# Optimization experiments

Hardware: AMD Instinct MI355X
Metric: run time of the kernel (lower is better)

## Reference

```python
import jax, jax.numpy as jnp
import numpy as np
import math

B, C, L = 8, 128, 8192
MODES = 512
TIME_DIM = 256
HIDDEN = 352  # SwiGLU: int(2*4*128/3)=341 rounded up to multiple of 16
EPS = 1e-6


def setup_inputs() -> dict:
    key = jax.random.key(0)
    ks = jax.random.split(key, 16)
    scale = 1.0 / (C * C)
    return {
        "x": jax.random.normal(ks[0], (B, C, L), jnp.float32),
        "t_emb": jax.random.normal(ks[1], (B, TIME_DIM), jnp.float32),
        "w_real": scale * jax.random.normal(ks[2], (C, C, MODES), jnp.float32),
        "w_imag": scale * jax.random.normal(ks[3], (C, C, MODES), jnp.float32),
        "shifts": 0.05 * jax.random.normal(ks[4], (C,), jnp.float32),
        "pw_w": jax.random.normal(ks[5], (C, C), jnp.float32) / math.sqrt(C),
        "pw_b": jnp.zeros((C,), jnp.float32),
        "dw_w": jax.random.normal(ks[6], (C, 3), jnp.float32) / math.sqrt(3.0),
        "dw_b": jnp.zeros((C,), jnp.float32),
        "norm_w": jnp.ones((C,), jnp.float32),
        "w1": jax.random.normal(ks[7], (HIDDEN, C), jnp.float32) / math.sqrt(C),
        "w2": jax.random.normal(ks[8], (HIDDEN, C), jnp.float32) / math.sqrt(C),
        "w3": jax.random.normal(ks[9], (C, HIDDEN), jnp.float32) / math.sqrt(HIDDEN),
        "tw": jax.random.normal(ks[10], (C, TIME_DIM), jnp.float32) / math.sqrt(TIME_DIM),
        "tb": jnp.zeros((C,), jnp.float32),
    }


def reference(x, t_emb, w_real, w_imag, shifts, pw_w, pw_b, dw_w, dw_b,
              norm_w, w1, w2, w3, tw, tb):
    Lx = x.shape[-1]
    nfreq = Lx // 2 + 1
    k = min(MODES, nfreq)
    residual = x

    # --- spectral path ---
    x_ft = jnp.fft.rfft(x, axis=-1)  # (B,C,nfreq) complex64
    w = (w_real + 1j * w_imag)[:, :, :k]  # (C,O,modes)
    w_spec = jnp.einsum('bcm,com->bom', x_ft[:, :, :k], w)
    # SpectralRoPE phase rotation
    freqs = jnp.arange(MODES, dtype=jnp.float32)[:k]
    theta = -2.0 * jnp.pi * shifts[:, None] * freqs[None, :]  # (C,k)
    rot = jnp.exp(1j * theta)
    w_spec = w_spec * rot[None]
    out_ft = jnp.concatenate([w_spec, x_ft[:, :, k:]], axis=-1) if nfreq > k else w_spec
    global_out = jnp.fft.irfft(out_ft, n=Lx, axis=-1)

    # --- local path: pointwise (1x1) + depthwise (k=3, pad=1) conv ---
    pw = jnp.einsum('bcl,oc->bol', x, pw_w) + pw_b[None, :, None]
    xp = jnp.pad(x, ((0, 0), (0, 0), (1, 1)))
    dw = (dw_w[None, :, 0:1] * xp[:, :, :-2]
          + dw_w[None, :, 1:2] * xp[:, :, 1:-1]
          + dw_w[None, :, 2:3] * xp[:, :, 2:]) + dw_b[None, :, None]
    h = global_out + pw + dw

    # --- time bias ---
    t_bias = jax.nn.silu(t_emb) @ tw.T + tb  # (B,C)
    h = h + t_bias[:, :, None]

    # --- RMSNorm + SwiGLU over channel dim ---
    h = h.transpose(0, 2, 1)  # (B,L,C)
    h = h * jax.lax.rsqrt(jnp.mean(h * h, axis=-1, keepdims=True) + EPS)
    h = h * norm_w
    h = (jax.nn.silu(h @ w1.T) * (h @ w2.T)) @ w3.T
    h = h.transpose(0, 2, 1)  # (B,C,L)
    return h + residual
```

## Files before the change

kernel.cpp:

```cpp
#include <hip/hip_runtime.h>
#include <hip/hip_bf16.h>
#include <math.h>

typedef short short8 __attribute__((ext_vector_type(8)));
typedef short short4v __attribute__((ext_vector_type(4)));
typedef float f32x4 __attribute__((ext_vector_type(4)));
typedef __bf16 bf16x8 __attribute__((ext_vector_type(8)));

#define DEVI __device__ __forceinline__

DEVI float bf2f(short u) {
  union { unsigned int u32; float f; } c;
  c.u32 = ((unsigned int)(unsigned short)u) << 16;
  return c.f;
}
DEVI short f2bf(float f) {
  __hip_bfloat16 h = __float2bfloat16(f);
  unsigned short u;
  __builtin_memcpy(&u, &h, 2);
  return (short)u;
}
DEVI f32x4 mfma16(bf16x8 a, bf16x8 b, f32x4 c) {
  return __builtin_amdgcn_mfma_f32_16x16x32_bf16(a, b, c, 0, 0, 0);
}

#define GLL16(gsrc, ldst) __builtin_amdgcn_global_load_lds( \
    (__attribute__((address_space(1))) void*)(gsrc), \
    (__attribute__((address_space(3))) void*)(ldst), 16, 0, 0)

__global__ __launch_bounds__(256) void k_prep_x(const float* __restrict__ x,
                                                short* __restrict__ xbf,
                                                short* __restrict__ xT) {
  __shared__ short T[64][66];
  int t = threadIdx.x;
  int lt = blockIdx.x & 127;
  int ct = (blockIdx.x >> 7) & 1;
  int b  = blockIdx.x >> 8;
  int c0 = ct << 6, l0 = lt << 6;
  int i = t >> 2, j4 = (t & 3) << 4;
  const float* src = x + (size_t)(b * 128 + c0 + i) * 8192 + l0 + j4;
  short hv[16];
#pragma unroll
  for (int e = 0; e < 16; e += 4) {
    float4 v = *(const float4*)(src + e);
    hv[e] = f2bf(v.x); hv[e + 1] = f2bf(v.y); hv[e + 2] = f2bf(v.z); hv[e + 3] = f2bf(v.w);
  }
  short8 o0, o1;
#pragma unroll
  for (int e = 0; e < 8; ++e) { o0[e] = hv[e]; o1[e] = hv[8 + e]; }
  short* dst = xbf + (size_t)(b * 128 + c0 + i) * 8192 + l0 + j4;
  *(short8*)dst = o0;
  *(short8*)(dst + 8) = o1;
#pragma unroll
  for (int e = 0; e < 16; ++e) T[i][j4 + e] = hv[e];
  __syncthreads();
  int jj = t >> 2, i4 = (t & 3) << 4;
  short8 p0, p1;
#pragma unroll
  for (int e = 0; e < 8; ++e) { p0[e] = T[i4 + e][jj]; p1[e] = T[i4 + 8 + e][jj]; }
  short* d2 = xT + ((size_t)b * 8192 + l0 + jj) * 128 + c0 + i4;
  *(short8*)d2 = p0;
  *(short8*)(d2 + 8) = p1;
}

__global__ __launch_bounds__(256) void k_prep_tf(short* __restrict__ tf) {
  int n = blockIdx.x >> 2;
  int l0 = ((blockIdx.x & 3) << 11) + (threadIdx.x << 3);
  int m = n >> 1;
  int odd = n & 1;
  short8 o;
#pragma unroll
  for (int e = 0; e < 8; ++e) {
    int l = l0 + e;
    int r = (m * l) & 8191;
    float s, c;
    sincospif((float)r * (1.0f / 4096.0f), &s, &c);
    o[e] = f2bf(odd ? -s : c);
  }
  *(short8*)(tf + (size_t)n * 8192 + l0) = o;
}

__global__ __launch_bounds__(256) void k_prep_ti(short* __restrict__ ti) {
  int l = blockIdx.x;
  int k0 = threadIdx.x << 2;
  short4v o;
#pragma unroll
  for (int e = 0; e < 4; ++e) {
    int k = k0 + e;
    int m = (k < 512) ? k : (k - 512);
    int r = (m * l) & 8191;
    float s, c;
    sincospif((float)r * (1.0f / 4096.0f), &s, &c);
    o[e] = f2bf((k < 512) ? c : s);
  }
  *(short4v*)(ti + (size_t)l * 1024 + k0) = o;
}

__global__ __launch_bounds__(256) void k_prep_w(const float* __restrict__ w1,
                                                const float* __restrict__ w2,
                                                const float* __restrict__ w3,
                                                const float* __restrict__ pw_w,
                                                short* __restrict__ w12,
                                                short* __restrict__ w3p,
                                                short* __restrict__ pwb) {
  int idx = blockIdx.x * 256 + threadIdx.x;
  if (idx < 98304) {
    int j = idx >> 7, c = idx & 127;
    float v = 0.f;
    if (j < 352) v = w1[j * 128 + c];
    else if (j >= 384 && j < 736) v = w2[(j - 384) * 128 + c];
    w12[idx] = f2bf(v);
  } else if (idx < 147456) {
    int q = idx - 98304;
    int o = q / 384, h = q - o * 384;
    w3p[q] = f2bf(h < 352 ? w3[o * 352 + h] : 0.f);
  } else if (idx < 163840) {
    int q = idx - 147456;
    pwb[q] = f2bf(pw_w[q]);
  }
}

__global__ __launch_bounds__(256) void k_prep_bias(const float* __restrict__ t_emb,
                                                   const float* __restrict__ tw,
                                                   const float* __restrict__ tb,
                                                   const float* __restrict__ pw_b,
                                                   const float* __restrict__ dw_b,
                                                   float* __restrict__ bias) {
  __shared__ float s[256];
  int b = blockIdx.x, t = threadIdx.x;
  float v = t_emb[b * 256 + t];
  s[t] = v / (1.0f + __expf(-v));
  __syncthreads();
  if (t < 128) {
    float acc = tb[t] + pw_b[t] + dw_b[t];
    for (int j = 0; j < 256; ++j) acc += s[j] * tw[t * 256 + j];
    bias[b * 128 + t] = acc;
  }
}

__global__ __launch_bounds__(256) void k_zero(float4* __restrict__ p, int n4) {
  int i = blockIdx.x * 256 + threadIdx.x;
  if (i < n4) p[i] = make_float4(0.f, 0.f, 0.f, 0.f);
}

__global__ __launch_bounds__(256, 2) void k_fwd(const short* __restrict__ A,
                                                const short* __restrict__ Bt,
                                                float* __restrict__ X) {
  __shared__ short As[2][4096];
  __shared__ short Bs[2][4096];
  int t = threadIdx.x;
  int nt = blockIdx.x & 7;
  int mt = (blockIdx.x >> 3) & 7;
  int kc = blockIdx.x >> 6;
  int lane = t & 63, wv = t >> 6;
  int wr = wv >> 1, wc = wv & 1;

  int rA = t >> 2, g = t & 3;
  int gs0 = (g ^ ((rA >> 1) & 3)) << 3;
  int rB = rA + 64;
  int gs1 = (g ^ ((rB >> 1) & 3)) << 3;

  const short* aS0 = A + (size_t)(mt * 128 + rA) * 8192 + kc * 1024 + gs0;
  const short* aS1 = A + (size_t)(mt * 128 + rB) * 8192 + kc * 1024 + gs1;
  const short* bS0 = Bt + (size_t)(nt * 128 + rA) * 8192 + kc * 1024 + gs0;
  const short* bS1 = Bt + (size_t)(nt * 128 + rB) * 8192 + kc * 1024 + gs1;

  f32x4 acc[4][4];
#pragma unroll
  for (int i = 0; i < 4; ++i)
#pragma unroll
    for (int j = 0; j < 4; ++j) acc[i][j] = (f32x4){0.f, 0.f, 0.f, 0.f};

  GLL16(aS0, &As[0][t * 8]);
  GLL16(aS1, &As[0][2048 + t * 8]);
  GLL16(bS0, &Bs[0][t * 8]);
  GLL16(bS1, &Bs[0][2048 + t * 8]);

  int rowk = lane & 15, kg = lane >> 4;

  for (int ks = 0; ks < 32; ++ks) {
    __syncthreads();
    int buf = ks & 1;
    if (ks + 1 < 32) {
      int ko = (ks + 1) * 32;
      GLL16(aS0 + ko, &As[buf ^ 1][t * 8]);
      GLL16(aS1 + ko, &As[buf ^ 1][2048 + t * 8]);
      GLL16(bS0 + ko, &Bs[buf ^ 1][t * 8]);
      GLL16(bS1 + ko, &Bs[buf ^ 1][2048 + t * 8]);
    }
    bf16x8 af[4], bfr[4];
#pragma unroll
    for (int fr = 0; fr < 4; ++fr) {
      int rr = wr * 64 + fr * 16 + rowk;
      int gg = kg ^ ((rr >> 1) & 3);
      af[fr] = *(const bf16x8*)(&As[buf][rr * 32 + gg * 8]);
    }
#pragma unroll
    for (int fc = 0; fc < 4; ++fc) {
      int rr = wc * 64 + fc * 16 + rowk;
      int gg = kg ^ ((rr >> 1) & 3);
      bfr[fc] = *(const bf16x8*)(&Bs[buf][rr * 32 + gg * 8]);
    }
#pragma unroll
    for (int fr = 0; fr < 4; ++fr)
#pragma unroll
      for (int fc = 0; fc < 4; ++fc)
        acc[fr][fc] = mfma16(af[fr], bfr[fc], acc[fr][fc]);
  }

  int rbase = mt * 128 + wr * 64 + (lane >> 4) * 4;
  int cbase = nt * 128 + wc * 64 + (lane & 15);
#pragma unroll
  for (int fr = 0; fr < 4; ++fr)
#pragma unroll
    for (int fc = 0; fc < 4; ++fc)
#pragma unroll
      for (int j = 0; j < 4; ++j)
        unsafeAtomicAdd(&X[(size_t)(rbase + fr * 16 + j) * 1024 + cbase + fc * 16],
                        acc[fr][fc][j]);
}

__global__ __launch_bounds__(256) void k_spec(const float* __restrict__ X,
                                              const float* __restrict__ wre,
                                              const float* __restrict__ wim,
                                              const float* __restrict__ shifts,
                                              short* __restrict__ D) {
  int t = threadIdx.x;
  int mt = blockIdx.x & 31, ot = blockIdx.x >> 5;
  int m = mt * 16 + (t & 15);
  int o = ot * 16 + (t >> 4);
  float ar[8], ai[8];
#pragma unroll
  for (int b = 0; b < 8; ++b) { ar[b] = 0.f; ai[b] = 0.f; }
  for (int c = 0; c < 128; ++c) {
    float wr = wre[((size_t)c * 128 + o) * 512 + m];
    float wi = wim[((size_t)c * 128 + o) * 512 + m];
#pragma unroll
    for (int b = 0; b < 8; ++b) {
      float2 xv = *(const float2*)(X + ((size_t)(b * 128 + c)) * 1024 + 2 * m);
      ar[b] += xv.x * wr - xv.y * wi;
      ai[b] += xv.x * wi + xv.y * wr;
    }
  }
  float phi = -6.283185307179586f * shifts[o] * (float)m;
  float sp, cp;
  sincosf(phi, &sp, &cp);
  float sc = (m == 0 ? 1.0f : 2.0f) * (1.0f / 8192.0f);
#pragma unroll
  for (int b = 0; b < 8; ++b) {
    float yr = ar[b] * cp - ai[b] * sp;
    float yi = ar[b] * sp + ai[b] * cp;
    float2 xo = *(const float2*)(X + ((size_t)(b * 128 + o)) * 1024 + 2 * m);
    D[((size_t)b * 128 + o) * 1024 + m]       = f2bf(sc * (yr - xo.x));
    D[((size_t)b * 128 + o) * 1024 + 512 + m] = f2bf(-sc * (yi - xo.y));
  }
}

__global__ __launch_bounds__(256, 2) void k_inv(const short* __restrict__ Ti,
                                                const short* __restrict__ D,
                                                const short* __restrict__ xT,
                                                const short* __restrict__ pwb,
                                                const float* __restrict__ dww,
                                                const float* __restrict__ bias,
                                                short* __restrict__ hp) {
  __shared__ short Sm[16384];
  __shared__ short xedge[256];
  short* As = Sm;
  short* Bs = Sm + 8192;
  int t = threadIdx.x;
  int lt = blockIdx.x & 63;
  int b  = blockIdx.x >> 6;
  int l0 = lt << 7;
  int lane = t & 63, wv = t >> 6;
  int wr = wv >> 1, wc = wv & 1;

  int rA = t >> 2, g = t & 3;
  int gs0 = (g ^ ((rA >> 1) & 3)) << 3;
  int rB = rA + 64;
  int gs1 = (g ^ ((rB >> 1) & 3)) << 3;

  const short* a1_0 = Ti + (size_t)(l0 + rA) * 1024 + gs0;
  const short* a1_1 = Ti + (size_t)(l0 + rB) * 1024 + gs1;
  const short* b1_0 = D + (size_t)(b * 128 + rA) * 1024 + gs0;
  const short* b1_1 = D + (size_t)(b * 128 + rB) * 1024 + gs1;
  const short* a2_0 = xT + ((size_t)b * 8192 + l0 + rA) * 128 + gs0;
  const short* a2_1 = xT + ((size_t)b * 8192 + l0 + rB) * 128 + gs1;
  const short* b2_0 = pwb + rA * 128 + gs0;
  const short* b2_1 = pwb + rB * 128 + gs1;

  f32x4 acc[4][4];
#pragma unroll
  for (int i = 0; i < 4; ++i)
#pragma unroll
    for (int j = 0; j < 4; ++j) acc[i][j] = (f32x4){0.f, 0.f, 0.f, 0.f};

  auto stage = [&](int buf, int ks) {
    int bo = buf * 4096;
    if (ks < 32) {
      int ko = ks * 32;
      GLL16(a1_0 + ko, &As[bo + t * 8]);
      GLL16(a1_1 + ko, &As[bo + 2048 + t * 8]);
      GLL16(b1_0 + ko, &Bs[bo + t * 8]);
      GLL16(b1_1 + ko, &Bs[bo + 2048 + t * 8]);
    } else {
      int ko = (ks - 32) * 32;
      GLL16(a2_0 + ko, &As[bo + t * 8]);
      GLL16(a2_1 + ko, &As[bo + 2048 + t * 8]);
      GLL16(b2_0 + ko, &Bs[bo + t * 8]);
      GLL16(b2_1 + ko, &Bs[bo + 2048 + t * 8]);
    }
  };

  stage(0, 0);
  int rowk = lane & 15, kg = lane >> 4;
  for (int ks = 0; ks < 36; ++ks) {
    __syncthreads();
    int buf = ks & 1;
    if (ks + 1 < 36) stage(buf ^ 1, ks + 1);
    bf16x8 af[4], bfr[4];
#pragma unroll
    for (int fr = 0; fr < 4; ++fr) {
      int rr = wr * 64 + fr * 16 + rowk;
      int gg = kg ^ ((rr >> 1) & 3);
      af[fr] = *(const bf16x8*)(&As[buf * 4096 + rr * 32 + gg * 8]);
    }
#pragma unroll
    for (int fc = 0; fc < 4; ++fc) {
      int rr = wc * 64 + fc * 16 + rowk;
      int gg = kg ^ ((rr >> 1) & 3);
      bfr[fc] = *(const bf16x8*)(&Bs[buf * 4096 + rr * 32 + gg * 8]);
    }
#pragma unroll
    for (int fr = 0; fr < 4; ++fr)
#pragma unroll
      for (int fc = 0; fc < 4; ++fc)
        acc[fr][fc] = mfma16(af[fr], bfr[fc], acc[fr][fc]);
  }

  __syncthreads();
  for (int i = t; i < 2080; i += 256) {
    if (i < 2048) {
      int row = i >> 4, seg = i & 15;
      short8 v = *(const short8*)(xT + ((size_t)b * 8192 + l0 + row) * 128 + seg * 8);
      *(short8*)(&Sm[row * 128 + seg * 8]) = v;
    } else {
      int e2 = i - 2048;
      int which = e2 >> 4, seg = e2 & 15;
      int l = which ? (l0 + 128) : (l0 - 1);
      short8 v = {0, 0, 0, 0, 0, 0, 0, 0};
      if (l >= 0 && l < 8192)
        v = *(const short8*)(xT + ((size_t)b * 8192 + l) * 128 + seg * 8);
      *(short8*)(&xedge[which * 128 + seg * 8]) = v;
    }
  }
  __syncthreads();

  const float* bb = bias + b * 128;
#pragma unroll
  for (int fc = 0; fc < 4; ++fc) {
    int o = wc * 64 + fc * 16 + rowk;
    float w0 = dww[o * 3], w1v = dww[o * 3 + 1], w2v = dww[o * 3 + 2];
    float bo = bb[o];
#pragma unroll
    for (int fr = 0; fr < 4; ++fr) {
#pragma unroll
      for (int j = 0; j < 4; ++j) {
        int ll = wr * 64 + fr * 16 + kg * 4 + j;
        float xm = (ll == 0)   ? bf2f(xedge[o])       : bf2f(Sm[(ll - 1) * 128 + o]);
        float x0 = bf2f(Sm[ll * 128 + o]);
        float xp = (ll == 127) ? bf2f(xedge[128 + o]) : bf2f(Sm[(ll + 1) * 128 + o]);
        float v = acc[fr][fc][j] + w0 * xm + w1v * x0 + w2v * xp + bo + x0;
        hp[((size_t)b * 8192 + l0 + ll) * 128 + o] = f2bf(v);
      }
    }
  }
}

__global__ __launch_bounds__(512, 2) void k_swi(const short* __restrict__ hp,
                                                const short* __restrict__ w12,
                                                const short* __restrict__ w3p,
                                                const float* __restrict__ normw,
                                                const float* __restrict__ x,
                                                float* __restrict__ out) {
  __shared__ short smem[32768];
  short* hA = smem;
  short* uA = smem + 8192;
  float* tr = (float*)smem;

  int t = threadIdx.x;
  int rb = blockIdx.x;
  int bb_ = rb >> 7;
  int l0 = (rb & 127) << 6;
  size_t row0 = (size_t)rb * 64;

  {
    int row = t >> 3, j = t & 7;
    const short* src = hp + (row0 + row) * 128 + j * 16;
    short8 v0 = *(const short8*)src;
    short8 v1 = *(const short8*)(src + 8);
    float f[16];
#pragma unroll
    for (int e = 0; e < 8; ++e) { f[e] = bf2f(v0[e]); f[8 + e] = bf2f(v1[e]); }
    float ss = 0.f;
#pragma unroll
    for (int e = 0; e < 16; ++e) ss += f[e] * f[e];
    ss += __shfl_xor(ss, 1);
    ss += __shfl_xor(ss, 2);
    ss += __shfl_xor(ss, 4);
    float rms = rsqrtf(ss * (1.0f / 128.0f) + 1e-6f);
    int cb = j * 16;
    short8 o0, o1;
#pragma unroll
    for (int e = 0; e < 8; ++e) {
      o0[e] = f2bf(f[e] * rms * normw[cb + e]);
      o1[e] = f2bf(f[8 + e] * rms * normw[cb + 8 + e]);
    }
    int g0 = (j * 2) ^ (row & 7);
    int g1 = (j * 2 + 1) ^ (row & 7);
    *(short8*)(&hA[row * 128 + g0 * 8]) = o0;
    *(short8*)(&hA[row * 128 + g1 * 8]) = o1;
  }
  __syncthreads();

  int lane = t & 63, wv = t >> 6;
  int wr = wv >> 2, wq = wv & 3;
  int rowk = lane & 15, kg = lane >> 4;

  f32x4 acc1[2][6], acc2[2][6];
#pragma unroll
  for (int i = 0; i < 2; ++i)
#pragma unroll
    for (int j = 0; j < 6; ++j) {
      acc1[i][j] = (f32x4){0.f, 0.f, 0.f, 0.f};
      acc2[i][j] = (f32x4){0.f, 0.f, 0.f, 0.f};
    }
#pragma unroll
  for (int ks = 0; ks < 4; ++ks) {
    bf16x8 a[2];
#pragma unroll
    for (int fr = 0; fr < 2; ++fr) {
      int rr = wr * 32 + fr * 16 + rowk;
      int gg = (ks * 4 + kg) ^ (rr & 7);
      a[fr] = *(const bf16x8*)(&hA[rr * 128 + gg * 8]);
    }
    int kk = ks * 32 + kg * 8;
#pragma unroll
    for (int fc = 0; fc < 6; ++fc) {
      int n = wq * 96 + fc * 16 + rowk;
      bf16x8 b1 = *(const bf16x8*)(w12 + (size_t)n * 128 + kk);
      bf16x8 b2 = *(const bf16x8*)(w12 + (size_t)(n + 384) * 128 + kk);
#pragma unroll
      for (int fr = 0; fr < 2; ++fr) {
        acc1[fr][fc] = mfma16(a[fr], b1, acc1[fr][fc]);
        acc2[fr][fc] = mfma16(a[fr], b2, acc2[fr][fc]);
      }
    }
  }
#pragma unroll
  for (int fr = 0; fr < 2; ++fr)
#pragma unroll
    for (int fc = 0; fc < 6; ++fc)
#pragma unroll
      for (int j = 0; j < 4; ++j) {
        float a1 = acc1[fr][fc][j], a2 = acc2[fr][fc][j];
        float u = a1 / (1.f + __expf(-a1)) * a2;
        int row = wr * 32 + fr * 16 + kg * 4 + j;
        int col = wq * 96 + fc * 16 + rowk;
        int cg = (col >> 3) ^ (row & 7);
        uA[row * 384 + cg * 8 + (col & 7)] = f2bf(u);
      }
  __syncthreads();

  f32x4 acc[2][2];
#pragma unroll
  for (int i = 0; i < 2; ++i)
#pragma unroll
    for (int j = 0; j < 2; ++j) acc[i][j] = (f32x4){0.f, 0.f, 0.f, 0.f};
#pragma unroll
  for (int ks = 0; ks < 12; ++ks) {
    bf16x8 a[2];
#pragma unroll
    for (int fr = 0; fr < 2; ++fr) {
      int rr = wr * 32 + fr * 16 + rowk;
      int gg = (ks * 4 + kg) ^ (rr & 7);
      a[fr] = *(const bf16x8*)(&uA[rr * 384 + gg * 8]);
    }
    int kk = ks * 32 + kg * 8;
#pragma unroll
    for (int fc = 0; fc < 2; ++fc) {
      int n = wq * 32 + fc * 16 + rowk;
      bf16x8 bw = *(const bf16x8*)(w3p + (size_t)n * 384 + kk);
#pragma unroll
      for (int fr = 0; fr < 2; ++fr) acc[fr][fc] = mfma16(a[fr], bw, acc[fr][fc]);
    }
  }
  __syncthreads();
#pragma unroll
  for (int fr = 0; fr < 2; ++fr)
#pragma unroll
    for (int fc = 0; fc < 2; ++fc)
#pragma unroll
      for (int j = 0; j < 4; ++j) {
        int r = wr * 32 + fr * 16 + kg * 4 + j;
        int c = wq * 32 + fc * 16 + rowk;
        tr[c * 65 + r] = acc[fr][fc][j];
      }
  __syncthreads();
  {
    int o = t >> 2, q = t & 3;
    const float* xs = x + ((size_t)(bb_ * 128 + o)) * 8192 + l0 + q * 16;
    float* os = out + ((size_t)(bb_ * 128 + o)) * 8192 + l0 + q * 16;
#pragma unroll
    for (int e4 = 0; e4 < 4; ++e4) {
      float4 xv = *(const float4*)(xs + e4 * 4);
      float4 r;
      r.x = tr[o * 65 + q * 16 + e4 * 4 + 0] + xv.x;
      r.y = tr[o * 65 + q * 16 + e4 * 4 + 1] + xv.y;
      r.z = tr[o * 65 + q * 16 + e4 * 4 + 2] + xv.z;
      r.w = tr[o * 65 + q * 16 + e4 * 4 + 3] + xv.w;
      *(float4*)(os + e4 * 4) = r;
    }
  }
}

extern "C" void kernel_launch(void* const* d_in, const int* in_sizes, int n_in,
                              void* d_out, int out_size, void* d_ws, size_t ws_size,
                              hipStream_t stream) {
  const float* x      = (const float*)d_in[0];
  const float* t_emb  = (const float*)d_in[1];
  const float* w_real = (const float*)d_in[2];
  const float* w_imag = (const float*)d_in[3];
  const float* shifts = (const float*)d_in[4];
  const float* pw_w   = (const float*)d_in[5];
  const float* pw_b   = (const float*)d_in[6];
  const float* dw_w   = (const float*)d_in[7];
  const float* dw_b   = (const float*)d_in[8];
  const float* norm_w = (const float*)d_in[9];
  const float* w1     = (const float*)d_in[10];
  const float* w2     = (const float*)d_in[11];
  const float* w3     = (const float*)d_in[12];
  const float* tw     = (const float*)d_in[13];
  const float* tb     = (const float*)d_in[14];
  float* out = (float*)d_out;
  char* ws = (char*)d_ws;

  short* xbf  = (short*)(ws + 0);
  short* xT   = (short*)(ws + 16777216);
  short* tf   = (short*)(ws + 33554432);
  short* ti   = (short*)(ws + 50331648);
  float* Xb   = (float*)(ws + 67108864);
  short* Db   = (short*)(ws + 71303168);
  short* hpre = (short*)(ws + 73400320);
  short* w12  = (short*)(ws + 90177536);
  short* w3p  = (short*)(ws + 90374144);
  short* pwb  = (short*)(ws + 90472448);
  float* bias = (float*)(ws + 90505216);

  k_prep_x<<<2048, 256, 0, stream>>>(x, xbf, xT);
  k_prep_tf<<<4096, 256, 0, stream>>>(tf);
  k_prep_ti<<<8192, 256, 0, stream>>>(ti);
  k_prep_w<<<640, 256, 0, stream>>>(w1, w2, w3, pw_w, w12, w3p, pwb);
  k_prep_bias<<<8, 256, 0, stream>>>(t_emb, tw, tb, pw_b, dw_b, bias);
  k_zero<<<1024, 256, 0, stream>>>((float4*)Xb, 262144);
  k_fwd<<<512, 256, 0, stream>>>(xbf, tf, Xb);
  k_spec<<<256, 256, 0, stream>>>(Xb, w_real, w_imag, shifts, Db);
  k_inv<<<512, 256, 0, stream>>>(ti, Db, xT, pwb, dw_w, bias, hpre);
  k_swi<<<1024, 512, 0, stream>>>(hpre, w12, w3p, norm_w, x, out);
}
```

Before: 452.8 us.

## Fuse RMSNorm into inverse kernel, split spectral mixing over channels, prelayout MLP weights

Three changes. The RMSNorm is moved into the epilogue of k_inv, with a cross-wave shared-memory row reduction, so k_swi can load the normalized tile straight into LDS with direct loads. The SwiGLU weights are pre-swizzled into MFMA fragment order, so each lane's B-operand load is contiguous. k_spec now runs 512 threads that split the channel reduction into two halves and combine them through shared memory, doubling parallelism for that latency-bound kernel. The costs are an extra barrier and added register pressure in k_inv.

New measurement: 404.8 us. 10.6% less time.

```diff
diff --git a/kernel.cpp b/kernel.cpp
--- a/kernel.cpp
+++ b/kernel.cpp
@@ -100,20 +100,28 @@
                                                 const float* __restrict__ w2,
                                                 const float* __restrict__ w3,
                                                 const float* __restrict__ pw_w,
-                                                short* __restrict__ w12,
-                                                short* __restrict__ w3p,
+                                                short* __restrict__ w12f,
+                                                short* __restrict__ w3f,
                                                 short* __restrict__ pwb) {
   int idx = blockIdx.x * 256 + threadIdx.x;
   if (idx < 98304) {
-    int j = idx >> 7, c = idx & 127;
+    int e = idx & 7, lane = (idx >> 3) & 63, ks = (idx >> 9) & 3, nt = idx >> 11;
+    int rowk = lane & 15, kg = lane >> 4;
+    int n = nt * 16 + rowk;
+    int k = ks * 32 + kg * 8 + e;
     float v = 0.f;
-    if (j < 352) v = w1[j * 128 + c];
-    else if (j >= 384 && j < 736) v = w2[(j - 384) * 128 + c];
-    w12[idx] = f2bf(v);
+    if (n < 352) v = w1[n * 128 + k];
+    else if (n >= 384 && n < 736) v = w2[(n - 384) * 128 + k];
+    w12f[idx] = f2bf(v);
   } else if (idx < 147456) {
     int q = idx - 98304;
-    int o = q / 384, h = q - o * 384;
-    w3p[q] = f2bf(h < 352 ? w3[o * 352 + h] : 0.f);
+    int e = q & 7, lane = (q >> 3) & 63;
+    int rest = q >> 9;
+    int nt = rest / 12, ks = rest - nt * 12;
+    int rowk = lane & 15, kg = lane >> 4;
+    int n = nt * 16 + rowk;
+    int k = ks * 32 + kg * 8 + e;
+    w3f[q] = f2bf(k < 352 ? w3[n * 352 + k] : 0.f);
   } else if (idx < 163840) {
     int q = idx - 147456;
     pwb[q] = f2bf(pw_w[q]);
@@ -220,39 +228,57 @@
                         acc[fr][fc][j]);
 }
 
-__global__ __launch_bounds__(256) void k_spec(const float* __restrict__ X,
+__global__ __launch_bounds__(512) void k_spec(const float* __restrict__ X,
                                               const float* __restrict__ wre,
                                               const float* __restrict__ wim,
                                               const float* __restrict__ shifts,
                                               short* __restrict__ D) {
+  __shared__ float red[16][256];
   int t = threadIdx.x;
+  int tt = t & 255;
+  int ch = t >> 8;
   int mt = blockIdx.x & 31, ot = blockIdx.x >> 5;
-  int m = mt * 16 + (t & 15);
-  int o = ot * 16 + (t >> 4);
+  int m = mt * 16 + (tt & 15);
+  int o = ot * 16 + (tt >> 4);
   float ar[8], ai[8];
 #pragma unroll
   for (int b = 0; b < 8; ++b) { ar[b] = 0.f; ai[b] = 0.f; }
-  for (int c = 0; c < 128; ++c) {
-    float wr = wre[((size_t)c * 128 + o) * 512 + m];
-    float wi = wim[((size_t)c * 128 + o) * 512 + m];
+  int cb = ch * 64;
+  const float* wrp = wre + (size_t)(cb * 128 + o) * 512 + m;
+  const float* wip = wim + (size_t)(cb * 128 + o) * 512 + m;
+  const float* Xp = X + 2 * m;
+#pragma unroll 4
+  for (int cc = 0; cc < 64; ++cc) {
+    float wr = wrp[(size_t)cc * 65536];
+    float wi = wip[(size_t)cc * 65536];
+    int c = cb + cc;
 #pragma unroll
     for (int b = 0; b < 8; ++b) {
-      float2 xv = *(const float2*)(X + ((size_t)(b * 128 + c)) * 1024 + 2 * m);
+      float2 xv = *(const float2*)(Xp + (size_t)(b * 128 + c) * 1024);
       ar[b] += xv.x * wr - xv.y * wi;
       ai[b] += xv.x * wi + xv.y * wr;
     }
   }
-  float phi = -6.283185307179586f * shifts[o] * (float)m;
-  float sp, cp;
-  sincosf(phi, &sp, &cp);
-  float sc = (m == 0 ? 1.0f : 2.0f) * (1.0f / 8192.0f);
-#pragma unroll
-  for (int b = 0; b < 8; ++b) {
-    float yr = ar[b] * cp - ai[b] * sp;
-    float yi = ar[b] * sp + ai[b] * cp;
-    float2 xo = *(const float2*)(X + ((size_t)(b * 128 + o)) * 1024 + 2 * m);
-    D[((size_t)b * 128 + o) * 1024 + m]       = f2bf(sc * (yr - xo.x));
-    D[((size_t)b * 128 + o) * 1024 + 512 + m] = f2bf(-sc * (yi - xo.y));
+  if (ch) {
+#pragma unroll
+    for (int b = 0; b < 8; ++b) { red[b * 2][tt] = ar[b]; red[b * 2 + 1][tt] = ai[b]; }
+  }
+  __syncthreads();
+  if (!ch) {
+#pragma unroll
+    for (int b = 0; b < 8; ++b) { ar[b] += red[b * 2][tt]; ai[b] += red[b * 2 + 1][tt]; }
+    float phi = -6.283185307179586f * shifts[o] * (float)m;
+    float sp, cp;
+    sincosf(phi, &sp, &cp);
+    float sc = (m == 0 ? 1.0f : 2.0f) * (1.0f / 8192.0f);
+#pragma unroll
+    for (int b = 0; b < 8; ++b) {
+      float yr = ar[b] * cp - ai[b] * sp;
+      float yi = ar[b] * sp + ai[b] * cp;
+      float2 xo = *(const float2*)(X + (size_t)(b * 128 + o) * 1024 + 2 * m);
+      D[((size_t)b * 128 + o) * 1024 + m]       = f2bf(sc * (yr - xo.x));
+      D[((size_t)b * 128 + o) * 1024 + 512 + m] = f2bf(-sc * (yi - xo.y));
+    }
   }
 }
 
@@ -262,9 +288,11 @@
                                                 const short* __restrict__ pwb,
                                                 const float* __restrict__ dww,
                                                 const float* __restrict__ bias,
-                                                short* __restrict__ hp) {
+                                                const float* __restrict__ nw,
+                                                short* __restrict__ hn) {
   __shared__ short Sm[16384];
   __shared__ short xedge[256];
+  __shared__ float rsS[2][128];
   short* As = Sm;
   short* Bs = Sm + 8192;
   int t = threadIdx.x;
@@ -369,17 +397,43 @@
         float xm = (ll == 0)   ? bf2f(xedge[o])       : bf2f(Sm[(ll - 1) * 128 + o]);
         float x0 = bf2f(Sm[ll * 128 + o]);
         float xp = (ll == 127) ? bf2f(xedge[128 + o]) : bf2f(Sm[(ll + 1) * 128 + o]);
-        float v = acc[fr][fc][j] + w0 * xm + w1v * x0 + w2v * xp + bo + x0;
-        hp[((size_t)b * 8192 + l0 + ll) * 128 + o] = f2bf(v);
+        acc[fr][fc][j] += w0 * xm + w1v * x0 + w2v * xp + bo + x0;
       }
     }
   }
-}
-
-__global__ __launch_bounds__(512, 2) void k_swi(const short* __restrict__ hp,
-                                                const short* __restrict__ w12,
-                                                const short* __restrict__ w3p,
-                                                const float* __restrict__ normw,
+#pragma unroll
+  for (int fr = 0; fr < 4; ++fr) {
+#pragma unroll
+    for (int j = 0; j < 4; ++j) {
+      float s = 0.f;
+#pragma unroll
+      for (int fc = 0; fc < 4; ++fc) { float v = acc[fr][fc][j]; s += v * v; }
+      s += __shfl_xor(s, 1);
+      s += __shfl_xor(s, 2);
+      s += __shfl_xor(s, 4);
+      s += __shfl_xor(s, 8);
+      if (rowk == 0) rsS[wc][wr * 64 + fr * 16 + kg * 4 + j] = s;
+    }
+  }
+  __syncthreads();
+#pragma unroll
+  for (int fr = 0; fr < 4; ++fr) {
+#pragma unroll
+    for (int j = 0; j < 4; ++j) {
+      int ll = wr * 64 + fr * 16 + kg * 4 + j;
+      float rms = rsqrtf((rsS[0][ll] + rsS[1][ll]) * (1.0f / 128.0f) + 1e-6f);
+#pragma unroll
+      for (int fc = 0; fc < 4; ++fc) {
+        int o = wc * 64 + fc * 16 + rowk;
+        hn[((size_t)b * 8192 + l0 + ll) * 128 + o] = f2bf(acc[fr][fc][j] * rms * nw[o]);
+      }
+    }
+  }
+}
+
+__global__ __launch_bounds__(512, 2) void k_swi(const short* __restrict__ hn,
+                                                const short* __restrict__ w12f,
+                                                const short* __restrict__ w3f,
                                                 const float* __restrict__ x,
                                                 float* __restrict__ out) {
   __shared__ short smem[32768];
@@ -388,41 +442,22 @@
   float* tr = (float*)smem;
 
   int t = threadIdx.x;
+  int lane = t & 63, wv = t >> 6;
   int rb = blockIdx.x;
   int bb_ = rb >> 7;
   int l0 = (rb & 127) << 6;
   size_t row0 = (size_t)rb * 64;
 
-  {
-    int row = t >> 3, j = t & 7;
-    const short* src = hp + (row0 + row) * 128 + j * 16;
-    short8 v0 = *(const short8*)src;
-    short8 v1 = *(const short8*)(src + 8);
-    float f[16];
-#pragma unroll
-    for (int e = 0; e < 8; ++e) { f[e] = bf2f(v0[e]); f[8 + e] = bf2f(v1[e]); }
-    float ss = 0.f;
-#pragma unroll
-    for (int e = 0; e < 16; ++e) ss += f[e] * f[e];
-    ss += __shfl_xor(ss, 1);
-    ss += __shfl_xor(ss, 2);
-    ss += __shfl_xor(ss, 4);
-    float rms = rsqrtf(ss * (1.0f / 128.0f) + 1e-6f);
-    int cb = j * 16;
-    short8 o0, o1;
-#pragma unroll
-    for (int e = 0; e < 8; ++e) {
-      o0[e] = f2bf(f[e] * rms * normw[cb + e]);
-      o1[e] = f2bf(f[8 + e] * rms * normw[cb + 8 + e]);
-    }
-    int g0 = (j * 2) ^ (row & 7);
-    int g1 = (j * 2 + 1) ^ (row & 7);
-    *(short8*)(&hA[row * 128 + g0 * 8]) = o0;
-    *(short8*)(&hA[row * 128 + g1 * 8]) = o1;
-  }
-  __syncthreads();
-
-  int lane = t & 63, wv = t >> 6;
+#pragma unroll
+  for (int c = 0; c < 2; ++c) {
+    int sidx = (wv * 2 + c) * 512 + lane * 8;
+    int row = sidx >> 7;
+    int g = (sidx >> 3) & 15;
+    const short* src = hn + (row0 + row) * 128 + (g ^ (row & 7)) * 8;
+    GLL16(src, &hA[sidx]);
+  }
+  __syncthreads();
+
   int wr = wv >> 2, wq = wv & 3;
   int rowk = lane & 15, kg = lane >> 4;
 
@@ -443,12 +478,11 @@
       int gg = (ks * 4 + kg) ^ (rr & 7);
       a[fr] = *(const bf16x8*)(&hA[rr * 128 + gg * 8]);
     }
-    int kk = ks * 32 + kg * 8;
 #pragma unroll
     for (int fc = 0; fc < 6; ++fc) {
-      int n = wq * 96 + fc * 16 + rowk;
-      bf16x8 b1 = *(const bf16x8*)(w12 + (size_t)n * 128 + kk);
-      bf16x8 b2 = *(const bf16x8*)(w12 + (size_t)(n + 384) * 128 + kk);
+      int nt = wq * 6 + fc;
+      bf16x8 b1 = *(const bf16x8*)(w12f + ((size_t)(nt * 4 + ks) * 64 + lane) * 8);
+      bf16x8 b2 = *(const bf16x8*)(w12f + ((size_t)((nt + 24) * 4 + ks) * 64 + lane) * 8);
 #pragma unroll
       for (int fr = 0; fr < 2; ++fr) {
         acc1[fr][fc] = mfma16(a[fr], b1, acc1[fr][fc]);
@@ -485,11 +519,10 @@
       int gg = (ks * 4 + kg) ^ (rr & 7);
       a[fr] = *(const bf16x8*)(&uA[rr * 384 + gg * 8]);
     }
-    int kk = ks * 32 + kg * 8;
 #pragma unroll
     for (int fc = 0; fc < 2; ++fc) {
-      int n = wq * 32 + fc * 16 + rowk;
-      bf16x8 bw = *(const bf16x8*)(w3p + (size_t)n * 384 + kk);
+      int nt = wq * 2 + fc;
+      bf16x8 bw = *(const bf16x8*)(w3f + ((size_t)(nt * 12 + ks) * 64 + lane) * 8);
 #pragma unroll
       for (int fr = 0; fr < 2; ++fr) acc[fr][fc] = mfma16(a[fr], bw, acc[fr][fc]);
     }
@@ -550,20 +583,20 @@
   short* ti   = (short*)(ws + 50331648);
   float* Xb   = (float*)(ws + 67108864);
   short* Db   = (short*)(ws + 71303168);
-  short* hpre = (short*)(ws + 73400320);
-  short* w12  = (short*)(ws + 90177536);
-  short* w3p  = (short*)(ws + 90374144);
+  short* hn   = (short*)(ws + 73400320);
+  short* w12f = (short*)(ws + 90177536);
+  short* w3f  = (short*)(ws + 90374144);
   short* pwb  = (short*)(ws + 90472448);
   float* bias = (float*)(ws + 90505216);
 
   k_prep_x<<<2048, 256, 0, stream>>>(x, xbf, xT);
   k_prep_tf<<<4096, 256, 0, stream>>>(tf);
   k_prep_ti<<<8192, 256, 0, stream>>>(ti);
-  k_prep_w<<<640, 256, 0, stream>>>(w1, w2, w3, pw_w, w12, w3p, pwb);
+  k_prep_w<<<640, 256, 0, stream>>>(w1, w2, w3, pw_w, w12f, w3f, pwb);
   k_prep_bias<<<8, 256, 0, stream>>>(t_emb, tw, tb, pw_b, dw_b, bias);
   k_zero<<<1024, 256, 0, stream>>>((float4*)Xb, 262144);
   k_fwd<<<512, 256, 0, stream>>>(xbf, tf, Xb);
-  k_spec<<<256, 256, 0, stream>>>(Xb, w_real, w_imag, shifts, Db);
-  k_inv<<<512, 256, 0, stream>>>(ti, Db, xT, pwb, dw_w, bias, hpre);
-  k_swi<<<1024, 512, 0, stream>>>(hpre, w12, w3p, norm_w, x, out);
-}
+  k_spec<<<256, 512, 0, stream>>>(Xb, w_real, w_imag, shifts, Db);
+  k_inv<<<512, 256, 0, stream>>>(ti, Db, xT, pwb, dw_w, bias, norm_w, hn);
+  k_swi<<<1024, 512, 0, stream>>>(hn, w12f, w3f, x, out);
+}
```
